# Kernel tuning notes

Measured on AMD Instinct MI355X. Metric: run time of the kernel, lower is better.

The kernel has to match this reference:

```python
import jax, jax.numpy as jnp
import numpy as np

H = 12  # num_heads

def setup_inputs() -> dict:
    key = jax.random.key(0)
    ks = jax.random.split(key, 6)
    B, L, D = 2, 2048, 768
    x = jax.random.normal(ks[0], (B, L, D), dtype=jnp.float32)
    token_sizes = jax.random.uniform(ks[1], (B, L), dtype=jnp.float32)
    attn_mask = jnp.triu(jnp.ones((L, L), dtype=bool), k=1)
    key_padding_mask = jnp.zeros((B, L), dtype=bool)
    qkv_w = jax.random.normal(ks[2], (3 * D, D), dtype=jnp.float32) * (D ** -0.5)
    qkv_b = jax.random.normal(ks[3], (3 * D,), dtype=jnp.float32) * 0.02
    proj_w = jax.random.normal(ks[4], (D, D), dtype=jnp.float32) * (D ** -0.5)
    proj_b = jax.random.normal(ks[5], (D,), dtype=jnp.float32) * 0.02
    return {"x": x, "token_sizes": token_sizes, "attn_mask": attn_mask,
            "key_padding_mask": key_padding_mask, "qkv_w": qkv_w, "qkv_b": qkv_b,
            "proj_w": proj_w, "proj_b": proj_b}

def reference(x, token_sizes, attn_mask, key_padding_mask, qkv_w, qkv_b, proj_w, proj_b):
    B, L, D = x.shape
    hd = D // H
    scale = hd ** -0.5
    qkv = (x @ qkv_w.T + qkv_b).reshape(B, L, 3, H, hd)
    qkv = jnp.transpose(qkv, (2, 0, 3, 1, 4))  # [3, B, H, L, hd]
    q, k, v = qkv[0], qkv[1], qkv[2]
    logits = jnp.einsum('bhqd,bhkd->bhqk', q, k) * scale  # [B,H,L,L]
    neg = jnp.finfo(logits.dtype).min
    logits = jnp.where(attn_mask[None, None, :, :], neg, logits)
    logits = jnp.where(key_padding_mask[:, None, None, :], neg, logits)
    logits = logits + jnp.log(jnp.clip(token_sizes, 1e-8))[:, None, None, :]
    attn = jax.nn.softmax(logits, axis=-1)
    out = jnp.einsum('bhqk,bhkd->bhqd', attn, v)
    out = jnp.transpose(out, (0, 2, 1, 3)).reshape(B, L, D)
    out = out @ proj_w.T + proj_b
    k_merge = k.mean(axis=1)  # [B, L, hd]
    return (out, k_merge)
```

## Files before the change

### kernel.cpp

```cpp
#include <hip/hip_runtime.h>
#include <hip/hip_bf16.h>

typedef unsigned short u16;
typedef __bf16 bf16x8 __attribute__((ext_vector_type(8)));
typedef float f32x4 __attribute__((ext_vector_type(4)));

#define QSCALE (0.125f * 1.44269504088896340736f)

__device__ __forceinline__ u16 f2bf(float f) {
    __hip_bfloat16 h = __float2bfloat16(f);
    return __builtin_bit_cast(u16, h);
}
__device__ __forceinline__ float bf2f(u16 u) {
    unsigned int x = ((unsigned int)u) << 16;
    return __builtin_bit_cast(float, x);
}
__device__ __forceinline__ bf16x8 ld_bf8(const u16* p) {
    uint4 u = *reinterpret_cast<const uint4*>(p);
    return __builtin_bit_cast(bf16x8, u);
}
__device__ __forceinline__ bf16x8 pack8f(f32x4 a, f32x4 b) {
    union { bf16x8 v; u16 u[8]; } r;
    #pragma unroll
    for (int i = 0; i < 4; i++) { r.u[i] = f2bf(a[i]); r.u[4+i] = f2bf(b[i]); }
    return r.v;
}
__device__ __forceinline__ bf16x8 pack8u(ushort4 a, ushort4 b) {
    union { bf16x8 v; ushort4 u[2]; } r;
    r.u[0] = a; r.u[1] = b;
    return r.v;
}

#define GLOAD_LDS16(g, l) __builtin_amdgcn_global_load_lds( \
    (const __attribute__((address_space(1))) unsigned int*)(g), \
    (__attribute__((address_space(3))) unsigned int*)(l), 16, 0, 0)

__global__ __launch_bounds__(256) void prep_kernel(
    const float* __restrict__ x, const float* __restrict__ qkvw,
    const float* __restrict__ projw, const float* __restrict__ ts,
    const unsigned char* __restrict__ kpm,
    u16* __restrict__ Xb, u16* __restrict__ Wq, u16* __restrict__ Wp,
    float* __restrict__ tsw, u16* __restrict__ tbf, int* __restrict__ qcount)
{
    int i = blockIdx.x * 256 + threadIdx.x;
    if (i == 0) *qcount = 0;
    const int XC4 = 4096 * 768 / 4;
    const int WQ4 = 2304 * 768 / 4;
    const int WP4 = 768 * 768 / 4;
    const float* src = nullptr; u16* dst = nullptr;
    if (i < XC4) { src = x; dst = Xb; }
    else {
        i -= XC4;
        if (i < WQ4) { src = qkvw; dst = Wq; }
        else {
            i -= WQ4;
            if (i < WP4) { src = projw; dst = Wp; }
            else {
                i -= WP4;
                if (i < 1024) {
                    float4 t = *(const float4*)(ts + i*4);
                    uchar4 k = *(const uchar4*)(kpm + i*4);
                    float4 r;
                    r.x = k.x ? 0.f : fmaxf(t.x, 1e-8f);
                    r.y = k.y ? 0.f : fmaxf(t.y, 1e-8f);
                    r.z = k.z ? 0.f : fmaxf(t.z, 1e-8f);
                    r.w = k.w ? 0.f : fmaxf(t.w, 1e-8f);
                    *(float4*)(tsw + i*4) = r;
                    ushort4 o;
                    o.x = f2bf(r.x); o.y = f2bf(r.y);
                    o.z = f2bf(r.z); o.w = f2bf(r.w);
                    *(ushort4*)(tbf + i*4) = o;
                }
                return;
            }
        }
    }
    float4 v = *(const float4*)(src + i*4);
    ushort4 o;
    o.x = f2bf(v.x); o.y = f2bf(v.y); o.z = f2bf(v.z); o.w = f2bf(v.w);
    *(ushort4*)(dst + i*4) = o;
}

template<int EPI>
__global__ __launch_bounds__(256) void gemm_bt(
    const u16* __restrict__ A, const u16* __restrict__ Bm,
    const float* __restrict__ bias, const float* __restrict__ tsw,
    u16* __restrict__ Qb, u16* __restrict__ Kb, u16* __restrict__ Vt,
    float* __restrict__ outp)
{
    __shared__ u16 As[2][128 * 32];
    __shared__ u16 Bs[2][128 * 32];
    const int K = 768;
    const int tid = threadIdx.x;
    const int nwg = gridDim.x * gridDim.y;
    const int flat = blockIdx.y * gridDim.x + blockIdx.x;
    const int per = nwg >> 3;
    const int swz = (flat & 7) * per + (flat >> 3);
    const int m0 = (swz / gridDim.x) * 128;
    const int n0 = (swz % gridDim.x) * 128;
    const int w = tid >> 6, lane = tid & 63;
    const int wr = (w >> 1) * 64, wc = (w & 1) * 64;
    const int g = lane >> 4, l16 = lane & 15;

    const int srow = lane >> 2;
    const int scol = (lane & 3) * 8;
    const u16* gA0 = A  + (size_t)(m0 + w*32      + srow) * K + scol;
    const u16* gA1 = A  + (size_t)(m0 + w*32 + 16 + srow) * K + scol;
    const u16* gB0 = Bm + (size_t)(n0 + w*32      + srow) * K + scol;
    const u16* gB1 = Bm + (size_t)(n0 + w*32 + 16 + srow) * K + scol;

#define GSTAGE(buf, kk) do { \
    GLOAD_LDS16(gA0 + (kk), &As[buf][(w*32     ) * 32]); \
    GLOAD_LDS16(gA1 + (kk), &As[buf][(w*32 + 16) * 32]); \
    GLOAD_LDS16(gB0 + (kk), &Bs[buf][(w*32     ) * 32]); \
    GLOAD_LDS16(gB1 + (kk), &Bs[buf][(w*32 + 16) * 32]); } while (0)

    f32x4 acc[4][4] = {};
    GSTAGE(0, 0);
    __syncthreads();
    for (int k0 = 0; k0 < K; k0 += 32) {
        const int cur = (k0 >> 5) & 1;
        if (k0 + 32 < K) GSTAGE(cur ^ 1, k0 + 32);
        bf16x8 af[4], bfr[4];
        #pragma unroll
        for (int i = 0; i < 4; i++) af[i]  = ld_bf8(&As[cur][(wr + i*16 + l16)*32 + g*8]);
        #pragma unroll
        for (int j = 0; j < 4; j++) bfr[j] = ld_bf8(&Bs[cur][(wc + j*16 + l16)*32 + g*8]);
        #pragma unroll
        for (int i = 0; i < 4; i++)
            #pragma unroll
            for (int j = 0; j < 4; j++)
                acc[i][j] = __builtin_amdgcn_mfma_f32_16x16x32_bf16(af[i], bfr[j], acc[i][j], 0, 0, 0);
        __syncthreads();
    }
#undef GSTAGE

    #pragma unroll
    for (int j = 0; j < 4; j++) {
        const int n = n0 + wc + j*16 + l16;
        const float bs = bias[n];
        #pragma unroll
        for (int i = 0; i < 4; i++) {
            #pragma unroll
            for (int r = 0; r < 4; r++) {
                const int m = m0 + wr + i*16 + g*4 + r;
                float v = acc[i][j][r] + bs;
                if (EPI == 0) {
                    int b = m >> 11, l = m & 2047;
                    unsigned int which = (unsigned int)n / 768u;
                    int rem = n - (int)which * 768;
                    int h = rem >> 6, d = rem & 63;
                    int bh = b * 12 + h;
                    if (which == 0)      Qb[((size_t)bh*2048 + l)*64 + d] = f2bf(v * QSCALE);
                    else if (which == 1) Kb[((size_t)bh*2048 + l)*64 + d] = f2bf(v);
                    else                 Vt[((size_t)bh*64 + d)*2048 + l] = f2bf(v * tsw[b*2048 + l]);
                } else {
                    outp[(size_t)m * 768 + n] = v;
                }
            }
        }
    }
}

__global__ __launch_bounds__(256, 2) void attn_kernel(
    const u16* __restrict__ Q, const u16* __restrict__ Kb,
    const u16* __restrict__ Vt, const u16* __restrict__ tbf,
    u16* __restrict__ O, int* __restrict__ qcount)
{
    __shared__ u16 Ks[2][64 * 64];
    __shared__ u16 Vs[2][64 * 64];
    __shared__ int s_item;
    const int tid = threadIdx.x;
    const int w = tid >> 6, lane = tid & 63;
    const int g = lane >> 4, l16 = lane & 15;
    const int sw = l16 & 7;
    const int srow = lane >> 3;
    const int sslot = (lane & 7) ^ srow;

    for (;;) {
        if (tid == 0) s_item = atomicAdd(qcount, 1);
        __syncthreads();
        const int item = s_item;
        if (item >= 768) return;
        const int qt = 31 - (item / 24);
        const int bh = item - (item / 24) * 24;
        const int b = bh / 12, h = bh - b * 12;
        const int q0 = qt * 64 + w * 16;
        const int nkt = qt + 1;

        const u16* Qp = Q + ((size_t)bh * 2048 + q0) * 64;
        const u16* Kp = Kb + (size_t)bh * 2048 * 64;
        const u16* Vp = Vt + (size_t)bh * 64 * 2048;
        const u16* tb = tbf + b * 2048;

        const u16* gK0 = Kp + (size_t)(w*16 +     srow) * 64   + sslot * 8;
        const u16* gK1 = Kp + (size_t)(w*16 + 8 + srow) * 64   + sslot * 8;
        const u16* gV0 = Vp + (size_t)(w*16 +     srow) * 2048 + sslot * 8;
        const u16* gV1 = Vp + (size_t)(w*16 + 8 + srow) * 2048 + sslot * 8;

#define ASTAGE(buf, kk) do { \
    GLOAD_LDS16(gK0 + (size_t)(kk) * 64, &Ks[buf][(w*16    ) * 64]); \
    GLOAD_LDS16(gK1 + (size_t)(kk) * 64, &Ks[buf][(w*16 + 8) * 64]); \
    GLOAD_LDS16(gV0 + (kk),              &Vs[buf][(w*16    ) * 64]); \
    GLOAD_LDS16(gV1 + (kk),              &Vs[buf][(w*16 + 8) * 64]); } while (0)

        const bf16x8 qf0 = ld_bf8(Qp + l16 * 64 + g * 8);
        const bf16x8 qf1 = ld_bf8(Qp + l16 * 64 + 32 + g * 8);

        f32x4 o[4] = {};
        f32x4 lpacc = {};
        float m = -1e30f;
        const int qmy = q0 + l16;

        ASTAGE(0, 0);
        __syncthreads();

        for (int kt = 0; kt < nkt; kt++) {
            const int cur = kt & 1;
            const int k0 = kt * 64;

            const u16* tp = tb + k0 + 4*g;
            ushort4 t0 = *(const ushort4*)(tp);
            ushort4 t1 = *(const ushort4*)(tp + 16);
            ushort4 t2 = *(const ushort4*)(tp + 32);
            ushort4 t3 = *(const ushort4*)(tp + 48);

            if (kt + 1 < nkt) ASTAGE(cur ^ 1, k0 + 64);

            const int ko0 = 8 * (g ^ sw);
            bf16x8 kf[4][2];
            #pragma unroll
            for (int t = 0; t < 4; t++) {
                const u16* kb = &Ks[cur][(t*16 + l16) * 64];
                kf[t][0] = ld_bf8(kb + ko0);
                kf[t][1] = ld_bf8(kb + (ko0 ^ 32));
            }
            const int gh = g >> 1, gl = 4 * (g & 1);
            ushort4 va[4][4];
            #pragma unroll
            for (int j = 0; j < 4; j++) {
                const u16* vb = &Vs[cur][(j*16 + l16) * 64];
                va[j][0] = *(const ushort4*)(vb + (((0 + gh) ^ sw) << 3) + gl);
                va[j][1] = *(const ushort4*)(vb + (((2 + gh) ^ sw) << 3) + gl);
                va[j][2] = *(const ushort4*)(vb + (((4 + gh) ^ sw) << 3) + gl);
                va[j][3] = *(const ushort4*)(vb + (((6 + gh) ^ sw) << 3) + gl);
            }

            f32x4 s[4];
            #pragma unroll
            for (int t = 0; t < 4; t++) {
                f32x4 z = {};
                z = __builtin_amdgcn_mfma_f32_16x16x32_bf16(kf[t][0], qf0, z, 0, 0, 0);
                z = __builtin_amdgcn_mfma_f32_16x16x32_bf16(kf[t][1], qf1, z, 0, 0, 0);
                s[t] = z;
            }
            if (kt == qt) {
                #pragma unroll
                for (int t = 0; t < 4; t++)
                    #pragma unroll
                    for (int r = 0; r < 4; r++) {
                        const int key = k0 + t*16 + 4*g + r;
                        if (key > qmy) s[t][r] = -1e30f;
                    }
            }
            float pmax = -1e30f;
            #pragma unroll
            for (int t = 0; t < 4; t++)
                #pragma unroll
                for (int r = 0; r < 4; r++)
                    pmax = fmaxf(pmax, s[t][r]);
            pmax = fmaxf(pmax, __shfl_xor(pmax, 16));
            pmax = fmaxf(pmax, __shfl_xor(pmax, 32));
            if (!__all(pmax <= m + 8.f)) {
                const float mn = fmaxf(m, pmax);
                const float sc = __builtin_amdgcn_exp2f(m - mn);
                m = mn;
                #pragma unroll
                for (int r = 0; r < 4; r++) {
                    const float scr = __shfl(sc, (lane & 48) + 4*g + r);
                    o[0][r] *= scr; o[1][r] *= scr; o[2][r] *= scr; o[3][r] *= scr;
                    lpacc[r] *= scr;
                }
            }
            #pragma unroll
            for (int t = 0; t < 4; t++)
                #pragma unroll
                for (int r = 0; r < 4; r++)
                    s[t][r] = __builtin_amdgcn_exp2f(s[t][r] - m);
            const bf16x8 pa01 = pack8f(s[0], s[1]);
            const bf16x8 pa23 = pack8f(s[2], s[3]);
            lpacc = __builtin_amdgcn_mfma_f32_16x16x32_bf16(pa01, pack8u(t0, t1), lpacc, 0, 0, 0);
            lpacc = __builtin_amdgcn_mfma_f32_16x16x32_bf16(pa23, pack8u(t2, t3), lpacc, 0, 0, 0);
            #pragma unroll
            for (int j = 0; j < 4; j++) {
                o[j] = __builtin_amdgcn_mfma_f32_16x16x32_bf16(pa01, pack8u(va[j][0], va[j][1]), o[j], 0, 0, 0);
                o[j] = __builtin_amdgcn_mfma_f32_16x16x32_bf16(pa23, pack8u(va[j][2], va[j][3]), o[j], 0, 0, 0);
            }
            __syncthreads();
        }
#undef ASTAGE

        float rlr[4];
        #pragma unroll
        for (int r = 0; r < 4; r++) rlr[r] = 1.f / lpacc[r];
        #pragma unroll
        for (int j = 0; j < 4; j++)
            #pragma unroll
            for (int r = 0; r < 4; r++) {
                const int q = q0 + 4*g + r;
                O[((size_t)b*2048 + q)*768 + h*64 + j*16 + l16] = f2bf(o[j][r] * rlr[r]);
            }
    }
}

__global__ __launch_bounds__(256) void kmerge_kernel(
    const u16* __restrict__ Kb, float* __restrict__ out)
{
    const int idx = blockIdx.x * 256 + threadIdx.x;
    const int d4 = (idx & 15) * 4;
    const int l = (idx >> 4) & 2047;
    const int b = idx >> 15;
    float4 acc = {0.f, 0.f, 0.f, 0.f};
    #pragma unroll
    for (int h = 0; h < 12; h++) {
        ushort4 v = *(const ushort4*)&Kb[(((size_t)(b*12 + h))*2048 + l)*64 + d4];
        acc.x += bf2f(v.x); acc.y += bf2f(v.y);
        acc.z += bf2f(v.z); acc.w += bf2f(v.w);
    }
    const float s = 1.f / 12.f;
    float4 r = {acc.x * s, acc.y * s, acc.z * s, acc.w * s};
    *(float4*)&out[(((size_t)b*2048 + l))*64 + d4] = r;
}

extern "C" void kernel_launch(void* const* d_in, const int* in_sizes, int n_in,
                              void* d_out, int out_size, void* d_ws, size_t ws_size,
                              hipStream_t stream)
{
    const float* x     = (const float*)d_in[0];
    const float* ts    = (const float*)d_in[1];
    const unsigned char* kpm = (const unsigned char*)d_in[3];
    const float* qkvw  = (const float*)d_in[4];
    const float* qkvb  = (const float*)d_in[5];
    const float* projw = (const float*)d_in[6];
    const float* projb = (const float*)d_in[7];
    float* out = (float*)d_out;

    char* ws = (char*)d_ws;
    u16* Xb = (u16*)ws;  ws += (size_t)4096 * 768 * 2;
    u16* Wq = (u16*)ws;  ws += (size_t)2304 * 768 * 2;
    u16* Wp = (u16*)ws;  ws += (size_t)768 * 768 * 2;
    u16* Qb = (u16*)ws;  ws += (size_t)24 * 2048 * 64 * 2;
    u16* Kb = (u16*)ws;  ws += (size_t)24 * 2048 * 64 * 2;
    u16* Vt = (u16*)ws;  ws += (size_t)24 * 2048 * 64 * 2;
    u16* Ob = (u16*)ws;  ws += (size_t)4096 * 768 * 2;
    float* tsw = (float*)ws;  ws += (size_t)2 * 2048 * 4;
    u16* tbf = (u16*)ws;  ws += (size_t)2 * 2048 * 2;
    int* qcount = (int*)ws;

    const int prep4 = (4096*768 + 2304*768 + 768*768) / 4 + 1024;
    prep_kernel<<<(prep4 + 255) / 256, 256, 0, stream>>>(
        x, qkvw, projw, ts, kpm, Xb, Wq, Wp, tsw, tbf, qcount);

    gemm_bt<0><<<dim3(18, 32), 256, 0, stream>>>(Xb, Wq, qkvb, tsw, Qb, Kb, Vt, nullptr);

    attn_kernel<<<dim3(512), 256, 0, stream>>>(Qb, Kb, Vt, tbf, Ob, qcount);

    kmerge_kernel<<<(2*2048*16) / 256, 256, 0, stream>>>(Kb, out + 3145728);

    gemm_bt<1><<<dim3(6, 32), 256, 0, stream>>>(Ob, Wp, projb, nullptr, nullptr, nullptr, nullptr, out);
}
```

Before: 110.7 us.

## Deepen GEMM and attention load pipelines with explicit waitcnt and barriers

Rewrites the GEMM main loop to keep two stages of global-to-LDS loads in flight. It uses explicit vmcnt waits and barriers in place of __syncthreads, and raises MFMA priority with setprio. The attention loop gets the same treatment: token-size loads are prefetched one tile ahead and synchronisation uses explicit wait counts. The output-projection GEMM switches to a 64-row tile to double its workgroup count, and launch bounds now request two blocks per CU. Hand-written waitcnt values are fragile: a miscount could cause races or stalls, and the smaller tile reduces data reuse.

```diff
diff --git a/kernel.cpp b/kernel.cpp
--- a/kernel.cpp
+++ b/kernel.cpp
@@ -34,6 +34,24 @@
 #define GLOAD_LDS16(g, l) __builtin_amdgcn_global_load_lds( \
     (const __attribute__((address_space(1))) unsigned int*)(g), \
     (__attribute__((address_space(3))) unsigned int*)(l), 16, 0, 0)
+
+template<int N> __device__ __forceinline__ void s_wait_vmcnt() {
+    if constexpr (N == 0)      asm volatile("s_waitcnt vmcnt(0)" ::: "memory");
+    else if constexpr (N == 3) asm volatile("s_waitcnt vmcnt(3)" ::: "memory");
+    else if constexpr (N == 4) asm volatile("s_waitcnt vmcnt(4)" ::: "memory");
+    else                       asm volatile("s_waitcnt vmcnt(8)" ::: "memory");
+}
+__device__ __forceinline__ void s_bar() {
+    __builtin_amdgcn_sched_barrier(0);
+    __builtin_amdgcn_s_barrier();
+    __builtin_amdgcn_sched_barrier(0);
+}
+__device__ __forceinline__ void s_wait_lgkm0_bar() {
+    asm volatile("s_waitcnt lgkmcnt(0)" ::: "memory");
+    __builtin_amdgcn_sched_barrier(0);
+    __builtin_amdgcn_s_barrier();
+    __builtin_amdgcn_sched_barrier(0);
+}
 
 __global__ __launch_bounds__(256) void prep_kernel(
     const float* __restrict__ x, const float* __restrict__ qkvw,
@@ -81,14 +99,18 @@
     *(ushort4*)(dst + i*4) = o;
 }
 
-template<int EPI>
-__global__ __launch_bounds__(256) void gemm_bt(
+template<int EPI, int MI>
+__global__ __launch_bounds__(256, 2) void gemm_bt(
     const u16* __restrict__ A, const u16* __restrict__ Bm,
     const float* __restrict__ bias, const float* __restrict__ tsw,
     u16* __restrict__ Qb, u16* __restrict__ Kb, u16* __restrict__ Vt,
     float* __restrict__ outp)
 {
-    __shared__ u16 As[2][128 * 32];
+    constexpr int BM = MI * 32;
+    constexpr int ACALLS = MI / 2;
+    constexpr int SA = ACALLS + 2;
+    constexpr int NT = 24;
+    __shared__ u16 As[2][BM * 32];
     __shared__ u16 Bs[2][128 * 32];
     const int K = 768;
     const int tid = threadIdx.x;
@@ -96,42 +118,54 @@
     const int flat = blockIdx.y * gridDim.x + blockIdx.x;
     const int per = nwg >> 3;
     const int swz = (flat & 7) * per + (flat >> 3);
-    const int m0 = (swz / gridDim.x) * 128;
+    const int m0 = (swz / gridDim.x) * BM;
     const int n0 = (swz % gridDim.x) * 128;
     const int w = tid >> 6, lane = tid & 63;
-    const int wr = (w >> 1) * 64, wc = (w & 1) * 64;
+    const int wr = (w >> 1) * (MI * 16), wc = (w & 1) * 64;
     const int g = lane >> 4, l16 = lane & 15;
 
     const int srow = lane >> 2;
     const int scol = (lane & 3) * 8;
-    const u16* gA0 = A  + (size_t)(m0 + w*32      + srow) * K + scol;
-    const u16* gA1 = A  + (size_t)(m0 + w*32 + 16 + srow) * K + scol;
-    const u16* gB0 = Bm + (size_t)(n0 + w*32      + srow) * K + scol;
-    const u16* gB1 = Bm + (size_t)(n0 + w*32 + 16 + srow) * K + scol;
+    const u16* gA[ACALLS];
+    #pragma unroll
+    for (int c = 0; c < ACALLS; c++)
+        gA[c] = A + (size_t)(m0 + (c*4 + w)*16 + srow) * K + scol;
+    const u16* gB[2];
+    #pragma unroll
+    for (int c = 0; c < 2; c++)
+        gB[c] = Bm + (size_t)(n0 + (c*4 + w)*16 + srow) * K + scol;
 
 #define GSTAGE(buf, kk) do { \
-    GLOAD_LDS16(gA0 + (kk), &As[buf][(w*32     ) * 32]); \
-    GLOAD_LDS16(gA1 + (kk), &As[buf][(w*32 + 16) * 32]); \
-    GLOAD_LDS16(gB0 + (kk), &Bs[buf][(w*32     ) * 32]); \
-    GLOAD_LDS16(gB1 + (kk), &Bs[buf][(w*32 + 16) * 32]); } while (0)
-
-    f32x4 acc[4][4] = {};
+    _Pragma("unroll") \
+    for (int c = 0; c < ACALLS; c++) \
+        GLOAD_LDS16(gA[c] + (kk), &As[buf][(c*4 + w) * 512]); \
+    _Pragma("unroll") \
+    for (int c = 0; c < 2; c++) \
+        GLOAD_LDS16(gB[c] + (kk), &Bs[buf][(c*4 + w) * 512]); } while (0)
+
+    f32x4 acc[MI][4] = {};
     GSTAGE(0, 0);
-    __syncthreads();
-    for (int k0 = 0; k0 < K; k0 += 32) {
-        const int cur = (k0 >> 5) & 1;
-        if (k0 + 32 < K) GSTAGE(cur ^ 1, k0 + 32);
-        bf16x8 af[4], bfr[4];
-        #pragma unroll
-        for (int i = 0; i < 4; i++) af[i]  = ld_bf8(&As[cur][(wr + i*16 + l16)*32 + g*8]);
-        #pragma unroll
-        for (int j = 0; j < 4; j++) bfr[j] = ld_bf8(&Bs[cur][(wc + j*16 + l16)*32 + g*8]);
-        #pragma unroll
-        for (int i = 0; i < 4; i++)
+    GSTAGE(1, 32);
+    for (int it = 0; it < NT; it++) {
+        const int k0 = it * 32;
+        const int cur = it & 1;
+        if (it < NT - 1) s_wait_vmcnt<SA>();
+        else             s_wait_vmcnt<0>();
+        s_bar();
+        bf16x8 af[MI], bfr[4];
+        #pragma unroll
+        for (int i = 0; i < MI; i++) af[i]  = ld_bf8(&As[cur][(wr + i*16 + l16)*32 + g*8]);
+        #pragma unroll
+        for (int j = 0; j < 4; j++)  bfr[j] = ld_bf8(&Bs[cur][(wc + j*16 + l16)*32 + g*8]);
+        s_wait_lgkm0_bar();
+        if (it + 2 < NT) GSTAGE(cur, k0 + 64);
+        __builtin_amdgcn_s_setprio(1);
+        #pragma unroll
+        for (int i = 0; i < MI; i++)
             #pragma unroll
             for (int j = 0; j < 4; j++)
                 acc[i][j] = __builtin_amdgcn_mfma_f32_16x16x32_bf16(af[i], bfr[j], acc[i][j], 0, 0, 0);
-        __syncthreads();
+        __builtin_amdgcn_s_setprio(0);
     }
 #undef GSTAGE
 
@@ -140,7 +174,7 @@
         const int n = n0 + wc + j*16 + l16;
         const float bs = bias[n];
         #pragma unroll
-        for (int i = 0; i < 4; i++) {
+        for (int i = 0; i < MI; i++) {
             #pragma unroll
             for (int r = 0; r < 4; r++) {
                 const int m = m0 + wr + i*16 + g*4 + r;
@@ -207,25 +241,32 @@
         const bf16x8 qf0 = ld_bf8(Qp + l16 * 64 + g * 8);
         const bf16x8 qf1 = ld_bf8(Qp + l16 * 64 + 32 + g * 8);
 
+        ushort4 tc0, tc1, tc2, tc3;
+        { const u16* tp = tb + 4*g;
+          tc0 = *(const ushort4*)(tp);      tc1 = *(const ushort4*)(tp + 16);
+          tc2 = *(const ushort4*)(tp + 32); tc3 = *(const ushort4*)(tp + 48); }
+        ASTAGE(0, 0);
+
         f32x4 o[4] = {};
         f32x4 lpacc = {};
         float m = -1e30f;
         const int qmy = q0 + l16;
 
-        ASTAGE(0, 0);
-        __syncthreads();
-
         for (int kt = 0; kt < nkt; kt++) {
             const int cur = kt & 1;
             const int k0 = kt * 64;
 
-            const u16* tp = tb + k0 + 4*g;
-            ushort4 t0 = *(const ushort4*)(tp);
-            ushort4 t1 = *(const ushort4*)(tp + 16);
-            ushort4 t2 = *(const ushort4*)(tp + 32);
-            ushort4 t3 = *(const ushort4*)(tp + 48);
-
-            if (kt + 1 < nkt) ASTAGE(cur ^ 1, k0 + 64);
+            ushort4 tn0 = tc0, tn1 = tc1, tn2 = tc2, tn3 = tc3;
+            if (kt + 1 < nkt) {
+                const u16* tp = tb + k0 + 64 + 4*g;
+                tn0 = *(const ushort4*)(tp);      tn1 = *(const ushort4*)(tp + 16);
+                tn2 = *(const ushort4*)(tp + 32); tn3 = *(const ushort4*)(tp + 48);
+                ASTAGE(cur ^ 1, k0 + 64);
+                s_wait_vmcnt<8>();
+            } else {
+                s_wait_vmcnt<0>();
+            }
+            s_bar();
 
             const int ko0 = 8 * (g ^ sw);
             bf16x8 kf[4][2];
@@ -289,14 +330,17 @@
                     s[t][r] = __builtin_amdgcn_exp2f(s[t][r] - m);
             const bf16x8 pa01 = pack8f(s[0], s[1]);
             const bf16x8 pa23 = pack8f(s[2], s[3]);
-            lpacc = __builtin_amdgcn_mfma_f32_16x16x32_bf16(pa01, pack8u(t0, t1), lpacc, 0, 0, 0);
-            lpacc = __builtin_amdgcn_mfma_f32_16x16x32_bf16(pa23, pack8u(t2, t3), lpacc, 0, 0, 0);
+            __builtin_amdgcn_s_setprio(1);
+            lpacc = __builtin_amdgcn_mfma_f32_16x16x32_bf16(pa01, pack8u(tc0, tc1), lpacc, 0, 0, 0);
+            lpacc = __builtin_amdgcn_mfma_f32_16x16x32_bf16(pa23, pack8u(tc2, tc3), lpacc, 0, 0, 0);
             #pragma unroll
             for (int j = 0; j < 4; j++) {
                 o[j] = __builtin_amdgcn_mfma_f32_16x16x32_bf16(pa01, pack8u(va[j][0], va[j][1]), o[j], 0, 0, 0);
                 o[j] = __builtin_amdgcn_mfma_f32_16x16x32_bf16(pa23, pack8u(va[j][2], va[j][3]), o[j], 0, 0, 0);
             }
-            __syncthreads();
+            __builtin_amdgcn_s_setprio(0);
+            s_wait_lgkm0_bar();
+            tc0 = tn0; tc1 = tn1; tc2 = tn2; tc3 = tn3;
         }
 #undef ASTAGE
 
@@ -361,11 +405,11 @@
     prep_kernel<<<(prep4 + 255) / 256, 256, 0, stream>>>(
         x, qkvw, projw, ts, kpm, Xb, Wq, Wp, tsw, tbf, qcount);
 
-    gemm_bt<0><<<dim3(18, 32), 256, 0, stream>>>(Xb, Wq, qkvb, tsw, Qb, Kb, Vt, nullptr);
+    gemm_bt<0, 4><<<dim3(18, 32), 256, 0, stream>>>(Xb, Wq, qkvb, tsw, Qb, Kb, Vt, nullptr);
 
     attn_kernel<<<dim3(512), 256, 0, stream>>>(Qb, Kb, Vt, tbf, Ob, qcount);
 
     kmerge_kernel<<<(2*2048*16) / 256, 256, 0, stream>>>(Kb, out + 3145728);
 
-    gemm_bt<1><<<dim3(6, 32), 256, 0, stream>>>(Ob, Wp, projb, nullptr, nullptr, nullptr, nullptr, out);
-}
+    gemm_bt<1, 2><<<dim3(6, 64), 256, 0, stream>>>(Ob, Wp, projb, nullptr, nullptr, nullptr, nullptr, out);
+}
```

Result: no change. 111.0 us (+0.3%).
